# Kernel optimization log

Measured on AMD Instinct MI355X. Metric: run time of the kernel, lower is better.

The kernel has to match this reference:

```python
import jax, jax.numpy as jnp
import numpy as np

N, C, H, W = 64, 512, 32, 32
HID, NCLS = 240, 10


def setup_inputs() -> dict:
    key = jax.random.key(0)
    ks = jax.random.split(key, 6)
    d = {
        "x": jax.random.normal(ks[0], (N, C, H, W), jnp.float32),
        "bn1_g": jnp.ones((C,), jnp.float32),
        "bn1_b": jnp.zeros((C,), jnp.float32),
        "bn1_m": jnp.zeros((C,), jnp.float32),
        "bn1_v": jnp.ones((C,), jnp.float32),
        "conv1_w": jax.random.normal(ks[1], (C, C, 3, 3), jnp.float32) * 0.02,
        "bn2_g": jnp.ones((C,), jnp.float32),
        "bn2_b": jnp.zeros((C,), jnp.float32),
        "bn2_m": jnp.zeros((C,), jnp.float32),
        "bn2_v": jnp.ones((C,), jnp.float32),
        "conv2_w": jax.random.normal(ks[2], (C, C, 3, 3), jnp.float32) * 0.02,
        "fc1_w": jax.random.normal(ks[3], (HID, C), jnp.float32) * 0.05,
        "fc1_b": jnp.zeros((HID,), jnp.float32),
        "fc2_w": jax.random.normal(ks[4], (NCLS, HID), jnp.float32) * 0.05,
        "fc2_b": jnp.zeros((NCLS,), jnp.float32),
    }
    return d


def _bn(x, g, b, m, v, eps=1e-5):
    # eval-mode BatchNorm2d, NCHW
    inv = g / jnp.sqrt(v + eps)
    return x * inv[None, :, None, None] + (b - m * inv)[None, :, None, None]


def _conv3(x, w):
    return jax.lax.conv_general_dilated(
        x, w, window_strides=(1, 1), padding="SAME",
        dimension_numbers=("NCHW", "OIHW", "NCHW"))


def _probe(feat, fc1_w, fc1_b, fc2_w, fc2_b):
    # Global_Avg_Flatten -> Linear -> Softplus(beta=5) -> Linear
    g = feat.mean(axis=(2, 3))                       # (N, C)
    h = jax.nn.softplus(5.0 * (g @ fc1_w.T + fc1_b)) / 5.0  # (N, HID)
    return h @ fc2_w.T + fc2_b                       # (N, NCLS)


def _get_mask(feat, fc1_w, fc1_b, fc2_w, fc2_b):
    # eval branch: sum of top-1 + top-2 logits, grad wrt (detached) feat
    feat_sg = jax.lax.stop_gradient(feat)

    def logit_sum(f_):
        logits = _probe(f_, fc1_w, fc1_b, fc2_w, fc2_b)
        idx = jax.lax.top_k(logits, 2)[1]            # (N, 2) int indices
        return jnp.take_along_axis(logits, idx, axis=1).sum()

    g = jax.grad(logit_sum)(feat_sg)                 # (N, C, H, W)
    # adaptive_avg_pool2d(.,1)*H*W == spatial sum
    s = g.sum(axis=(2, 3))                           # (N, C)
    m = jax.nn.softmax(s, axis=1) * 2.0
    return m[:, :, None, None]


def reference(x, bn1_g, bn1_b, bn1_m, bn1_v, conv1_w,
              bn2_g, bn2_b, bn2_m, bn2_v, conv2_w,
              fc1_w, fc1_b, fc2_w, fc2_b):
    out1 = jax.nn.relu(_bn(x, bn1_g, bn1_b, bn1_m, bn1_v))  # equalInOut path
    mask = _get_mask(out1, fc1_w, fc1_b, fc2_w, fc2_b)
    pred_probe = _probe(out1, fc1_w, fc1_b, fc2_w, fc2_b)
    masked = out1 * mask
    h = jax.nn.relu(_bn(_conv3(masked, conv1_w), bn2_g, bn2_b, bn2_m, bn2_v))
    h = _conv3(h, conv2_w)
    out = x + h
    return (out, pred_probe)
```

## Files before the change

kernel.cpp:

```cpp
#include <hip/hip_runtime.h>
#include <stdint.h>

typedef __bf16 bf16x8 __attribute__((ext_vector_type(8)));
typedef float f32x4v __attribute__((ext_vector_type(4)));

typedef __attribute__((address_space(1))) const void gconst_t;
typedef __attribute__((address_space(3))) void lds_t;

#define GLL16(gp, sp) __builtin_amdgcn_global_load_lds((gconst_t*)(uintptr_t)(gp), (lds_t*)(uintptr_t)(sp), 16, 0, 0)

__device__ __forceinline__ unsigned short f2bf(float f) {
  unsigned int u = __float_as_uint(f);
  u = (u + 0x7FFFu + ((u >> 16) & 1u)) >> 16;
  return (unsigned short)u;
}
__device__ __forceinline__ float bf2f(unsigned int b) {
  return __uint_as_float(b << 16);
}

#define SPP 1156

__global__ __launch_bounds__(512) void bnprep(
    const float* __restrict__ g1, const float* __restrict__ b1,
    const float* __restrict__ m1, const float* __restrict__ v1,
    const float* __restrict__ g2, const float* __restrict__ b2,
    const float* __restrict__ m2, const float* __restrict__ v2,
    float* __restrict__ bnp) {
  int t = threadIdx.x;
  float i1 = g1[t] * rsqrtf(v1[t] + 1e-5f);
  bnp[t] = i1;
  bnp[512 + t] = b1[t] - m1[t] * i1;
  float i2 = g2[t] * rsqrtf(v2[t] + 1e-5f);
  bnp[1024 + t] = i2;
  bnp[1536 + t] = b2[t] - m2[t] * i2;
}

__global__ __launch_bounds__(256) void ring_zero(unsigned short* __restrict__ Ap,
                                                 unsigned short* __restrict__ Hp) {
  const int n = blockIdx.y;
  const int p = blockIdx.x * 4 + (threadIdx.x >> 6);
  const int lane = threadIdx.x & 63;
  int y, x;
  if (p < 34) { y = 0; x = p; }
  else if (p < 68) { y = 33; x = p - 34; }
  else if (p < 100) { y = p - 67; x = 0; }
  else { y = p - 99; x = 33; }
  const uint4 z = {0u, 0u, 0u, 0u};
  const size_t off = ((size_t)((n * 34 + y) * 34 + x)) * 512 + lane * 8;
  *(uint4*)(Ap + off) = z;
  *(uint4*)(Hp + off) = z;
}

__global__ __launch_bounds__(256) void wtrans(const float* __restrict__ w1, const float* __restrict__ w2,
                                              unsigned short* __restrict__ w1t, unsigned short* __restrict__ w2t) {
  unsigned e = blockIdx.x * 256u + threadIdx.x;
  if (e >= 4718592u) return;
  const float* w = (e < 2359296u) ? w1 : w2;
  unsigned short* o = (e < 2359296u) ? w1t : w2t;
  unsigned r = (e < 2359296u) ? e : (e - 2359296u);
  unsigned ci = r & 511u, co = (r >> 9) & 511u, tt = r >> 18;
  o[r] = f2bf(w[(co * 512u + ci) * 9u + tt]);
}

__global__ __launch_bounds__(256) void bn1_relu_stage(const float* __restrict__ x, const float* __restrict__ bnp,
                                                      unsigned short* __restrict__ Ap, float* __restrict__ partial) {
  int bid = blockIdx.x;
  int n = bid >> 6, ciblk = (bid >> 3) & 7, yblk = bid & 7;
  int ci0 = ciblk * 64, y0 = yblk * 4;
  int t = threadIdx.x;
  __shared__ __align__(16) float vals[64 * 128];
  __shared__ float ivs[64], bbs[64];
  if (t < 64) { ivs[t] = bnp[ci0 + t]; bbs[t] = bnp[512 + ci0 + t]; }
  __syncthreads();
#pragma unroll
  for (int i = 0; i < 8; ++i) {
    int f4 = i * 256 + t;
    int cil = f4 >> 5, xq = f4 & 31;
    const float* src = x + ((size_t)(n * 512 + ci0 + cil)) * 1024 + y0 * 32 + xq * 4;
    f32x4v v = *(const f32x4v*)src;
    float iv = ivs[cil], bb = bbs[cil];
    f32x4v r;
    r[0] = fmaxf(fmaf(v[0], iv, bb), 0.f);
    r[1] = fmaxf(fmaf(v[1], iv, bb), 0.f);
    r[2] = fmaxf(fmaf(v[2], iv, bb), 0.f);
    r[3] = fmaxf(fmaf(v[3], iv, bb), 0.f);
    *(f32x4v*)&vals[cil * 128 + xq * 4] = r;
  }
  __syncthreads();
  {
    int cil = t >> 2, q = t & 3;
    float s = 0.f;
#pragma unroll
    for (int j = 0; j < 32; ++j) s += vals[cil * 128 + q * 32 + j];
    s += __shfl_xor(s, 1);
    s += __shfl_xor(s, 2);
    if (q == 0) partial[((size_t)n * 512 + ci0 + cil) * 8 + yblk] = s;
  }
  {
    int yx = t >> 1, half = t & 1;
    int y = y0 + (yx >> 5), xx = yx & 31;
    unsigned short* dp = Ap + ((size_t)((n * 34 + y + 1) * 34 + (xx + 1))) * 512 + ci0 + half * 32;
    unsigned wrd[16];
#pragma unroll
    for (int j = 0; j < 16; ++j) {
      unsigned lo = f2bf(vals[(half * 32 + 2 * j) * 128 + yx]);
      unsigned hi = f2bf(vals[(half * 32 + 2 * j + 1) * 128 + yx]);
      wrd[j] = lo | (hi << 16);
    }
#pragma unroll
    for (int k = 0; k < 4; ++k) {
      uint4 u;
      u.x = wrd[k * 4]; u.y = wrd[k * 4 + 1]; u.z = wrd[k * 4 + 2]; u.w = wrd[k * 4 + 3];
      *(uint4*)(dp + k * 8) = u;
    }
  }
}

__global__ __launch_bounds__(256) void probe_mask(const float* __restrict__ partial,
                                                  const float* __restrict__ fc1w, const float* __restrict__ fc1b,
                                                  const float* __restrict__ fc2w, const float* __restrict__ fc2b,
                                                  float* __restrict__ maskp, float* __restrict__ probeout) {
  int n = blockIdx.x, t = threadIdx.x;
  int lane = t & 63, wv = t >> 6;
  __shared__ float gl[512], sl[512], zl[240], hl[240], dzl[240], logl[10], red[4];
  __shared__ int idx2[2];
  for (int c = t; c < 512; c += 256) {
    const float* pp = partial + ((size_t)n * 512 + c) * 8;
    float s = 0.f;
#pragma unroll
    for (int j = 0; j < 8; ++j) s += pp[j];
    gl[c] = s * (1.f / 1024.f);
  }
  __syncthreads();
  if (t < 240) {
    float z = fc1b[t];
    const float* wr = fc1w + t * 512;
    for (int c = 0; c < 512; ++c) z = fmaf(gl[c], wr[c], z);
    zl[t] = z;
    float u = 5.f * z;
    float sp = (u > 20.f) ? u : log1pf(expf(u));
    hl[t] = sp * 0.2f;
  }
  __syncthreads();
  if (t < 10) {
    float L = fc2b[t];
    const float* wr = fc2w + t * 240;
    for (int h = 0; h < 240; ++h) L = fmaf(hl[h], wr[h], L);
    logl[t] = L;
    probeout[n * 10 + t] = L;
  }
  __syncthreads();
  if (t == 0) {
    float b1v = -1e30f, b2v = -1e30f; int i1 = 0, i2 = 0;
    for (int j = 0; j < 10; ++j) {
      float v = logl[j];
      if (v > b1v) { b2v = b1v; i2 = i1; b1v = v; i1 = j; }
      else if (v > b2v) { b2v = v; i2 = j; }
    }
    idx2[0] = i1; idx2[1] = i2;
  }
  __syncthreads();
  if (t < 240) {
    float dh = fc2w[idx2[0] * 240 + t] + fc2w[idx2[1] * 240 + t];
    float u = 5.f * zl[t];
    float sg = 1.f / (1.f + expf(-u));
    dzl[t] = dh * sg;
  }
  __syncthreads();
  for (int c = t; c < 512; c += 256) {
    float s = 0.f;
    for (int h = 0; h < 240; ++h) s = fmaf(dzl[h], fc1w[h * 512 + c], s);
    sl[c] = s;
  }
  __syncthreads();
  float m = fmaxf(sl[t], sl[t + 256]);
#pragma unroll
  for (int o = 32; o > 0; o >>= 1) m = fmaxf(m, __shfl_xor(m, o));
  if (lane == 0) red[wv] = m;
  __syncthreads();
  float mx = fmaxf(fmaxf(red[0], red[1]), fmaxf(red[2], red[3]));
  float e0 = expf(sl[t] - mx), e1 = expf(sl[t + 256] - mx);
  float sum = e0 + e1;
#pragma unroll
  for (int o = 32; o > 0; o >>= 1) sum += __shfl_xor(sum, o);
  __syncthreads();
  if (lane == 0) red[wv] = sum;
  __syncthreads();
  float inv = 2.f / (red[0] + red[1] + red[2] + red[3]);
  maskp[(size_t)n * 512 + t] = e0 * inv;
  maskp[(size_t)n * 512 + t + 256] = e1 * inv;
}

#define LT(M) ((l4 ^ (((M) + l7) & 7)) << 4)

#define RD_A2(QM, H, TAP) do {                                                \
  const int _S0 = ((QM) * 2 + (H) + (TAP) / 3) * 34 + (TAP) % 3;              \
  const int _l = l15x128 + LT(_S0 & 7);                                       \
  const char* _p = ldsAW + _S0 * 128;                                         \
  a2[0][0] = *(const bf16x8*)(_p + _l);                                       \
  a2[0][1] = *(const bf16x8*)(_p + (_l ^ 64));                                \
  a2[1][0] = *(const bf16x8*)(_p + 2048 + _l);                                \
  a2[1][1] = *(const bf16x8*)(_p + 2048 + (_l ^ 64));                         \
} while (0)

#define RD_B(BUF) do {                                                        \
  const char* _pb = ldsb + 49152 + (BUF) * 16384;                             \
  b[0][0] = *(const bf16x8*)(_pb + bRdC);                                     \
  b[0][1] = *(const bf16x8*)(_pb + (bRdC ^ 64));                              \
  b[1][0] = *(const bf16x8*)(_pb + 2048 + bRdC);                              \
  b[1][1] = *(const bf16x8*)(_pb + 2048 + (bRdC ^ 64));                       \
} while (0)

#define ST_B(BUF, BP) do {                                                    \
  GLL16((BP) + bOff0,         ldsb + 49152 + (BUF) * 16384 + tb);             \
  GLL16((BP) + bOff0 + 32768, ldsb + 49152 + (BUF) * 16384 + 8192 + tb);      \
} while (0)

#define ST_A3(AP) do {                                                        \
  GLL16((AP) + aOff0,          ldsb + tb);                                    \
  GLL16((AP) + aOff0 + 32768,  ldsb + 8192 + tb);                             \
  GLL16((AP) + aOff0 + 65536,  ldsb + 16384 + tb);                            \
  GLL16((AP) + aOff0 + 98304,  ldsb + 24576 + tb);                            \
  GLL16((AP) + aOff0 + 131072, ldsb + 32768 + tb);                            \
  GLL16((AP) + aOff0 + 163840, ldsb + 40960 + tb);                            \
} while (0)

#define RMW_A(CIB) do {                                                       \
  const float* _mp = maskp + (size_t)n * 512 + (CIB) * 64 + kq8;              \
  const f32x4v _m0 = *(const f32x4v*)_mp;                                     \
  const f32x4v _m1 = *(const f32x4v*)(_mp + 4);                               \
  _Pragma("unroll") for (int r = 0; r < 6; ++r) {                             \
    char* _pp = ldsb + tb + r * 8192;                                         \
    bf16x8 _v = *(bf16x8*)_pp;                                                \
    bf16x8 _o;                                                                \
    _o[0] = (__bf16)((float)_v[0] * _m0[0]);                                  \
    _o[1] = (__bf16)((float)_v[1] * _m0[1]);                                  \
    _o[2] = (__bf16)((float)_v[2] * _m0[2]);                                  \
    _o[3] = (__bf16)((float)_v[3] * _m0[3]);                                  \
    _o[4] = (__bf16)((float)_v[4] * _m1[0]);                                  \
    _o[5] = (__bf16)((float)_v[5] * _m1[1]);                                  \
    _o[6] = (__bf16)((float)_v[6] * _m1[2]);                                  \
    _o[7] = (__bf16)((float)_v[7] * _m1[3]);                                  \
    *(bf16x8*)_pp = _o;                                                       \
  }                                                                           \
} while (0)

#define MFMA8(QM, H) do {                                                     \
  _Pragma("unroll") for (int m = 0; m < 2; ++m)                               \
  _Pragma("unroll") for (int n2 = 0; n2 < 2; ++n2) {                          \
    acc[QM][(H) * 2 + m][n2] = __builtin_amdgcn_mfma_f32_16x16x32_bf16(       \
        a2[m][0], b[n2][0], acc[QM][(H) * 2 + m][n2], 0, 0, 0);               \
    acc[QM][(H) * 2 + m][n2] = __builtin_amdgcn_mfma_f32_16x16x32_bf16(       \
        a2[m][1], b[n2][1], acc[QM][(H) * 2 + m][n2], 0, 0, 0); }             \
} while (0)

#define BARR __builtin_amdgcn_s_barrier()
#define LGKM0 do { asm volatile("s_waitcnt lgkmcnt(0)" ::: "memory");         \
                   __builtin_amdgcn_sched_barrier(0); } while (0)
#define VM0 asm volatile("s_waitcnt vmcnt(0)" ::: "memory")
#define PRIO1 __builtin_amdgcn_s_setprio(1)
#define PRIO0 __builtin_amdgcn_s_setprio(0)

#define TAPSTEP(TAP, PAR) do {                                                \
  const unsigned short* _bpn;                                                 \
  if ((TAP) < 8) _bpn = Wt + (size_t)((TAP) + 1) * 262144 + k8 * 64;          \
  else           _bpn = (k8 < 7) ? Wt + (size_t)(k8 + 1) * 64                 \
                                 : Wt + (size_t)8 * 262144 + 7 * 64;          \
  ST_B((((TAP) + (PAR)) & 1) ^ 1, _bpn);                                      \
  RD_B(((TAP) + (PAR)) & 1);                                                  \
  RD_A2(0, 0, TAP); PRIO1; MFMA8(0, 0); PRIO0;                                \
  RD_A2(0, 1, TAP); PRIO1; MFMA8(0, 1); PRIO0;                                \
  RD_A2(1, 0, TAP); PRIO1; MFMA8(1, 0); PRIO0;                                \
  if ((TAP) < 8) {                                                            \
    RD_A2(1, 1, TAP); PRIO1; MFMA8(1, 1); PRIO0;                              \
    VM0; LGKM0; BARR;                                                         \
  } else {                                                                    \
    RD_A2(1, 1, TAP);                                                         \
    LGKM0; BARR;                                                              \
    if (k8 < 7) { ST_A3(Ag + (size_t)(k8 + 1) * 64); }                        \
    PRIO1; MFMA8(1, 1); PRIO0;                                                \
    VM0; BARR;                                                                \
    if (MODE == 1 && k8 < 7) {                                                \
      RMW_A(k8 + 1);                                                          \
      LGKM0; BARR;                                                            \
    }                                                                         \
  }                                                                           \
} while (0)

#define TAP9(PAR)                                                             \
  TAPSTEP(0, PAR); TAPSTEP(1, PAR); TAPSTEP(2, PAR);                          \
  TAPSTEP(3, PAR); TAPSTEP(4, PAR); TAPSTEP(5, PAR);                          \
  TAPSTEP(6, PAR); TAPSTEP(7, PAR); TAPSTEP(8, PAR);

template <int MODE>
__global__ __attribute__((amdgpu_flat_work_group_size(512, 512), amdgpu_waves_per_eu(4, 4)))
void conv256(
    const unsigned short* __restrict__ Ain,
    const unsigned short* __restrict__ Wt,
    const float* __restrict__ bnp,
    const float* __restrict__ maskp,
    unsigned short* __restrict__ Hout,
    const float* __restrict__ xres,
    float* __restrict__ outp) {
  __shared__ __align__(16) char ldsb[81920];

  const int t = threadIdx.x;
  const int lane = t & 63;
  const int wv = t >> 6;
  const int wm = wv >> 2;
  const int wn = wv & 3;

  const int bid = blockIdx.x;
  const int logical = (bid & 7) * 128 + (bid >> 3);
  const int nt = logical & 3, mt = logical >> 2;
  const int n = mt >> 2, yblk = mt & 3;
  const int co0 = nt * 128;

  const unsigned short* Ag = Ain + (size_t)n * (SPP * 512);

  const int kq8 = ((t & 7) ^ ((t >> 3) & 7)) * 8;
  const int aOff0 = (yblk * 272 + (t >> 3)) * 512 + kq8;
  const int bOff0 = (co0 + (t >> 3)) * 512 + kq8;
  const int tb = t * 16;
  const int l4 = lane >> 4, l7 = lane & 7;
  const int l15x128 = (lane & 15) * 128;
  const char* ldsAW = ldsb + wm * 17408;
  const int bRdC = (wn * 32 + (lane & 15)) * 128 + (((lane >> 4) ^ (lane & 7)) << 4);

  bf16x8 a2[2][2];
  bf16x8 b[2][2];
  f32x4v acc[2][4][2];
  const f32x4v zero = {0.f, 0.f, 0.f, 0.f};
#pragma unroll
  for (int qm = 0; qm < 2; ++qm)
#pragma unroll
    for (int mi = 0; mi < 4; ++mi)
#pragma unroll
      for (int ni = 0; ni < 2; ++ni) acc[qm][mi][ni] = zero;

  {
    ST_A3(Ag);
    ST_B(0, Wt);
    VM0; BARR;
    if (MODE == 1) {
      RMW_A(0);
      LGKM0; BARR;
    }
  }

  for (int k2 = 0; k2 < 4; ++k2) {
    {
      const int k8 = 2 * k2;
      TAP9(0)
    }
    {
      const int k8 = 2 * k2 + 1;
      TAP9(1)
    }
  }
  VM0;
  __syncthreads();

  if constexpr (MODE == 1) {
#pragma unroll
    for (int ni = 0; ni < 2; ++ni) {
      const int cog = co0 + wn * 32 + ni * 16 + (lane & 15);
      const float iv = bnp[1024 + cog];
      const float bb = bnp[1536 + cog];
#pragma unroll
      for (int qm = 0; qm < 2; ++qm)
#pragma unroll
        for (int mi = 0; mi < 4; ++mi)
#pragma unroll
          for (int r = 0; r < 4; ++r) {
            const int row = wm * 128 + qm * 64 + mi * 16 + (lane >> 4) * 4 + r;
            const int y = yblk * 8 + (row >> 5), xx = row & 31;
            const float v = fmaxf(fmaf(acc[qm][mi][ni][r], iv, bb), 0.f);
            Hout[((size_t)((n * 34 + y + 1) * 34 + (xx + 1))) * 512 + cog] = f2bf(v);
          }
    }
  } else {
    float* sm = (float*)ldsb;
    const int spat0 = yblk * 256;
#pragma unroll 1
    for (int h = 0; h < 4; ++h) {
      if (wn == h) {
#pragma unroll
        for (int ni = 0; ni < 2; ++ni)
#pragma unroll
          for (int qm = 0; qm < 2; ++qm)
#pragma unroll
            for (int mi = 0; mi < 4; ++mi)
#pragma unroll
              for (int r = 0; r < 4; ++r)
                sm[(ni * 16 + (lane & 15)) * 264 +
                   wm * 128 + qm * 64 + mi * 16 + (lane >> 4) * 4 + r] = acc[qm][mi][ni][r];
      }
      __syncthreads();
#pragma unroll
      for (int j = 0; j < 4; ++j) {
        const int c = j * 512 + t;
        const int cc = c >> 6, px = (c & 63) * 4;
        f32x4v v = *(const f32x4v*)&sm[cc * 264 + px];
        const int cog = co0 + h * 32 + cc;
        const size_t o = ((size_t)(n * 512 + cog)) * 1024 + spat0 + px;
        const f32x4v xr = *(const f32x4v*)(xres + o);
        v = v + xr;
        *(f32x4v*)(outp + o) = v;
      }
      __syncthreads();
    }
  }
}

extern "C" void kernel_launch(void* const* d_in, const int* in_sizes, int n_in,
                              void* d_out, int out_size, void* d_ws, size_t ws_size,
                              hipStream_t stream) {
  (void)in_sizes; (void)n_in; (void)out_size; (void)ws_size;
  const float* x    = (const float*)d_in[0];
  const float* bn1g = (const float*)d_in[1];
  const float* bn1b = (const float*)d_in[2];
  const float* bn1m = (const float*)d_in[3];
  const float* bn1v = (const float*)d_in[4];
  const float* w1   = (const float*)d_in[5];
  const float* bn2g = (const float*)d_in[6];
  const float* bn2b = (const float*)d_in[7];
  const float* bn2m = (const float*)d_in[8];
  const float* bn2v = (const float*)d_in[9];
  const float* w2   = (const float*)d_in[10];
  const float* fc1w = (const float*)d_in[11];
  const float* fc1b = (const float*)d_in[12];
  const float* fc2w = (const float*)d_in[13];
  const float* fc2b = (const float*)d_in[14];

  float* out = (float*)d_out;
  float* probeo = out + (size_t)64 * 512 * 32 * 32;

  char* ws = (char*)d_ws;
  unsigned short* Ap  = (unsigned short*)(ws);
  unsigned short* Hp  = (unsigned short*)(ws + 75759616);
  unsigned short* W1t = (unsigned short*)(ws + 151519232);
  unsigned short* W2t = (unsigned short*)(ws + 156237824);
  float* partial      = (float*)(ws + 160956416);
  float* maskp        = (float*)(ws + 162004992);
  float* bnp          = (float*)(ws + 162136064);

  bnprep<<<1, 512, 0, stream>>>(bn1g, bn1b, bn1m, bn1v, bn2g, bn2b, bn2m, bn2v, bnp);
  ring_zero<<<dim3(33, 64), 256, 0, stream>>>(Ap, Hp);
  wtrans<<<18432, 256, 0, stream>>>(w1, w2, W1t, W2t);
  bn1_relu_stage<<<4096, 256, 0, stream>>>(x, bnp, Ap, partial);
  probe_mask<<<64, 256, 0, stream>>>(partial, fc1w, fc1b, fc2w, fc2b, maskp, probeo);
  conv256<1><<<1024, 512, 0, stream>>>(Ap, W1t, bnp, maskp, Hp, nullptr, nullptr);
  conv256<2><<<1024, 512, 0, stream>>>(Hp, W2t, bnp, nullptr, nullptr, x, out);
}
```

Before: 586.6 us.

## Reshape conv wave tiling from 2x4 to 4x2 waves with 64x64 per-wave tiles

Changes the per-wave output tile in the implicit-GEMM conv from 128 pixels by 32 channels (2x4 wave grid) to 64 pixels by 64 channels (4x2 wave grid). All four A fragments are loaded once per tap, then B fragments are streamed per 16-channel slice. This balances A/B reuse and lowers LDS read traffic per MFMA. The swizzle and epilogue indexing are reworked to match. It risks different register pressure and scheduling, and the new swizzle may cause LDS bank conflicts.

```diff
diff --git a/kernel.cpp b/kernel.cpp
--- a/kernel.cpp
+++ b/kernel.cpp
@@ -191,24 +191,36 @@
   maskp[(size_t)n * 512 + t + 256] = e1 * inv;
 }
 
-#define LT(M) ((l4 ^ (((M) + l7) & 7)) << 4)
-
-#define RD_A2(QM, H, TAP) do {                                                \
-  const int _S0 = ((QM) * 2 + (H) + (TAP) / 3) * 34 + (TAP) % 3;              \
-  const int _l = l15x128 + LT(_S0 & 7);                                       \
-  const char* _p = ldsAW + _S0 * 128;                                         \
-  a2[0][0] = *(const bf16x8*)(_p + _l);                                       \
-  a2[0][1] = *(const bf16x8*)(_p + (_l ^ 64));                                \
-  a2[1][0] = *(const bf16x8*)(_p + 2048 + _l);                                \
-  a2[1][1] = *(const bf16x8*)(_p + 2048 + (_l ^ 64));                         \
-} while (0)
-
-#define RD_B(BUF) do {                                                        \
-  const char* _pb = ldsb + 49152 + (BUF) * 16384;                             \
-  b[0][0] = *(const bf16x8*)(_pb + bRdC);                                     \
-  b[0][1] = *(const bf16x8*)(_pb + (bRdC ^ 64));                              \
-  b[1][0] = *(const bf16x8*)(_pb + 2048 + bRdC);                              \
-  b[1][1] = *(const bf16x8*)(_pb + 2048 + (bRdC ^ 64));                       \
+#define BARR __builtin_amdgcn_s_barrier()
+#define LGKM0 do { asm volatile("s_waitcnt lgkmcnt(0)" ::: "memory");         \
+                   __builtin_amdgcn_sched_barrier(0); } while (0)
+#define VM0 asm volatile("s_waitcnt vmcnt(0)" ::: "memory")
+#define PRIO1 __builtin_amdgcn_s_setprio(1)
+#define PRIO0 __builtin_amdgcn_s_setprio(0)
+
+#define SBL(MF, TAP) (((((MF) >> 1) + (TAP) / 3) * 34) + ((TAP) % 3) + 16 * ((MF) & 1))
+
+#define RD_A_ALL(TAP) do {                                                    \
+  _Pragma("unroll") for (int mf = 0; mf < 4; ++mf) {                          \
+    const int _sb = SBL(mf, TAP);                                             \
+    const int _ad = wmBase + _sb * 128 + aTw[_sb & 7];                        \
+    a4[mf][0] = *(const bf16x8*)(ldsb + _ad);                                 \
+    a4[mf][1] = *(const bf16x8*)(ldsb + (_ad ^ 64));                          \
+  }                                                                           \
+} while (0)
+
+#define RD_B1(NF, BUF) do {                                                   \
+  const int _bd = 49152 + (BUF) * 16384 + (NF) * 2048 + bRdC;                 \
+  b2[0] = *(const bf16x8*)(ldsb + _bd);                                       \
+  b2[1] = *(const bf16x8*)(ldsb + (_bd ^ 64));                                \
+} while (0)
+
+#define MFMA_NF(NF) do {                                                      \
+  _Pragma("unroll") for (int mf = 0; mf < 4; ++mf) {                          \
+    acc[mf][NF] = __builtin_amdgcn_mfma_f32_16x16x32_bf16(                    \
+        a4[mf][0], b2[0], acc[mf][NF], 0, 0, 0);                              \
+    acc[mf][NF] = __builtin_amdgcn_mfma_f32_16x16x32_bf16(                    \
+        a4[mf][1], b2[1], acc[mf][NF], 0, 0, 0); }                            \
 } while (0)
 
 #define ST_B(BUF, BP) do {                                                    \
@@ -245,40 +257,24 @@
   }                                                                           \
 } while (0)
 
-#define MFMA8(QM, H) do {                                                     \
-  _Pragma("unroll") for (int m = 0; m < 2; ++m)                               \
-  _Pragma("unroll") for (int n2 = 0; n2 < 2; ++n2) {                          \
-    acc[QM][(H) * 2 + m][n2] = __builtin_amdgcn_mfma_f32_16x16x32_bf16(       \
-        a2[m][0], b[n2][0], acc[QM][(H) * 2 + m][n2], 0, 0, 0);               \
-    acc[QM][(H) * 2 + m][n2] = __builtin_amdgcn_mfma_f32_16x16x32_bf16(       \
-        a2[m][1], b[n2][1], acc[QM][(H) * 2 + m][n2], 0, 0, 0); }             \
-} while (0)
-
-#define BARR __builtin_amdgcn_s_barrier()
-#define LGKM0 do { asm volatile("s_waitcnt lgkmcnt(0)" ::: "memory");         \
-                   __builtin_amdgcn_sched_barrier(0); } while (0)
-#define VM0 asm volatile("s_waitcnt vmcnt(0)" ::: "memory")
-#define PRIO1 __builtin_amdgcn_s_setprio(1)
-#define PRIO0 __builtin_amdgcn_s_setprio(0)
-
 #define TAPSTEP(TAP, PAR) do {                                                \
   const unsigned short* _bpn;                                                 \
   if ((TAP) < 8) _bpn = Wt + (size_t)((TAP) + 1) * 262144 + k8 * 64;          \
   else           _bpn = (k8 < 7) ? Wt + (size_t)(k8 + 1) * 64                 \
                                  : Wt + (size_t)8 * 262144 + 7 * 64;          \
   ST_B((((TAP) + (PAR)) & 1) ^ 1, _bpn);                                      \
-  RD_B(((TAP) + (PAR)) & 1);                                                  \
-  RD_A2(0, 0, TAP); PRIO1; MFMA8(0, 0); PRIO0;                                \
-  RD_A2(0, 1, TAP); PRIO1; MFMA8(0, 1); PRIO0;                                \
-  RD_A2(1, 0, TAP); PRIO1; MFMA8(1, 0); PRIO0;                                \
+  RD_A_ALL(TAP);                                                              \
+  RD_B1(0, ((TAP) + (PAR)) & 1); PRIO1; MFMA_NF(0); PRIO0;                    \
+  RD_B1(1, ((TAP) + (PAR)) & 1); PRIO1; MFMA_NF(1); PRIO0;                    \
+  RD_B1(2, ((TAP) + (PAR)) & 1); PRIO1; MFMA_NF(2); PRIO0;                    \
   if ((TAP) < 8) {                                                            \
-    RD_A2(1, 1, TAP); PRIO1; MFMA8(1, 1); PRIO0;                              \
+    RD_B1(3, ((TAP) + (PAR)) & 1); PRIO1; MFMA_NF(3); PRIO0;                  \
     VM0; LGKM0; BARR;                                                         \
   } else {                                                                    \
-    RD_A2(1, 1, TAP);                                                         \
+    RD_B1(3, ((TAP) + (PAR)) & 1);                                            \
     LGKM0; BARR;                                                              \
     if (k8 < 7) { ST_A3(Ag + (size_t)(k8 + 1) * 64); }                        \
-    PRIO1; MFMA8(1, 1); PRIO0;                                                \
+    PRIO1; MFMA_NF(3); PRIO0;                                                 \
     VM0; BARR;                                                                \
     if (MODE == 1 && k8 < 7) {                                                \
       RMW_A(k8 + 1);                                                          \
@@ -307,8 +303,11 @@
   const int t = threadIdx.x;
   const int lane = t & 63;
   const int wv = t >> 6;
-  const int wm = wv >> 2;
-  const int wn = wv & 3;
+  const int wm = wv >> 1;
+  const int wn = wv & 1;
+  const int l15 = lane & 15;
+  const int l4 = lane >> 4;
+  const int l7 = lane & 7;
 
   const int bid = blockIdx.x;
   const int logical = (bid & 7) * 128 + (bid >> 3);
@@ -322,21 +321,22 @@
   const int aOff0 = (yblk * 272 + (t >> 3)) * 512 + kq8;
   const int bOff0 = (co0 + (t >> 3)) * 512 + kq8;
   const int tb = t * 16;
-  const int l4 = lane >> 4, l7 = lane & 7;
-  const int l15x128 = (lane & 15) * 128;
-  const char* ldsAW = ldsb + wm * 17408;
-  const int bRdC = (wn * 32 + (lane & 15)) * 128 + (((lane >> 4) ^ (lane & 7)) << 4);
-
-  bf16x8 a2[2][2];
-  bf16x8 b[2][2];
-  f32x4v acc[2][4][2];
+
+  int aTw[8];
+#pragma unroll
+  for (int m = 0; m < 8; ++m)
+    aTw[m] = l15 * 128 + ((l4 ^ ((m + 4 * wm + l7) & 7)) << 4);
+  const int wmBase = wm * 8704;
+  const int bRdC = (wn * 64 + l15) * 128 + ((l4 ^ l7) << 4);
+
+  bf16x8 a4[4][2];
+  bf16x8 b2[2];
+  f32x4v acc[4][4];
   const f32x4v zero = {0.f, 0.f, 0.f, 0.f};
 #pragma unroll
-  for (int qm = 0; qm < 2; ++qm)
-#pragma unroll
-    for (int mi = 0; mi < 4; ++mi)
-#pragma unroll
-      for (int ni = 0; ni < 2; ++ni) acc[qm][mi][ni] = zero;
+  for (int mf = 0; mf < 4; ++mf)
+#pragma unroll
+    for (int nf = 0; nf < 4; ++nf) acc[mf][nf] = zero;
 
   {
     ST_A3(Ag);
@@ -363,38 +363,36 @@
 
   if constexpr (MODE == 1) {
 #pragma unroll
-    for (int ni = 0; ni < 2; ++ni) {
-      const int cog = co0 + wn * 32 + ni * 16 + (lane & 15);
+    for (int nf = 0; nf < 4; ++nf) {
+      const int cog = co0 + wn * 64 + nf * 16 + l15;
       const float iv = bnp[1024 + cog];
       const float bb = bnp[1536 + cog];
 #pragma unroll
-      for (int qm = 0; qm < 2; ++qm)
-#pragma unroll
-        for (int mi = 0; mi < 4; ++mi)
-#pragma unroll
-          for (int r = 0; r < 4; ++r) {
-            const int row = wm * 128 + qm * 64 + mi * 16 + (lane >> 4) * 4 + r;
-            const int y = yblk * 8 + (row >> 5), xx = row & 31;
-            const float v = fmaxf(fmaf(acc[qm][mi][ni][r], iv, bb), 0.f);
-            Hout[((size_t)((n * 34 + y + 1) * 34 + (xx + 1))) * 512 + cog] = f2bf(v);
-          }
+      for (int mf = 0; mf < 4; ++mf) {
+        const int y = yblk * 8 + 2 * wm + (mf >> 1);
+        unsigned short* hb = Hout + ((size_t)((n * 34 + y + 1) * 34 + 1)) * 512 + cog;
+#pragma unroll
+        for (int r = 0; r < 4; ++r) {
+          const int xx = (mf & 1) * 16 + l4 * 4 + r;
+          hb[(size_t)xx * 512] = f2bf(fmaxf(fmaf(acc[mf][nf][r], iv, bb), 0.f));
+        }
+      }
     }
   } else {
     float* sm = (float*)ldsb;
     const int spat0 = yblk * 256;
 #pragma unroll 1
     for (int h = 0; h < 4; ++h) {
-      if (wn == h) {
-#pragma unroll
-        for (int ni = 0; ni < 2; ++ni)
-#pragma unroll
-          for (int qm = 0; qm < 2; ++qm)
-#pragma unroll
-            for (int mi = 0; mi < 4; ++mi)
-#pragma unroll
-              for (int r = 0; r < 4; ++r)
-                sm[(ni * 16 + (lane & 15)) * 264 +
-                   wm * 128 + qm * 64 + mi * 16 + (lane >> 4) * 4 + r] = acc[qm][mi][ni][r];
+      if (wn == (h >> 1)) {
+#pragma unroll
+        for (int q = 0; q < 2; ++q) {
+          const int nf = 2 * (h & 1) + q;
+#pragma unroll
+          for (int mf = 0; mf < 4; ++mf)
+#pragma unroll
+            for (int r = 0; r < 4; ++r)
+              sm[(q * 16 + l15) * 264 + wm * 64 + mf * 16 + l4 * 4 + r] = acc[mf][nf][r];
+        }
       }
       __syncthreads();
 #pragma unroll
```

Result: slower. 1.079 ms (+83.9%).
